# Kernel optimization log

Hardware: AMD Instinct MI355X
Metric: run time of the kernel (lower is better)

The kernel has to match this reference:

```python
import jax, jax.numpy as jnp
import numpy as np

N = 100_000   # nodes
E = 1_600_000 # edges per relation (avg degree 16)
IN, H, O = 128, 128, 128


def _graph_conv(x, src, dst, W, b, relu):
    """DGL GraphConv, norm='both': y = D_dst^{-1/2} A D_src^{-1/2} x W + b."""
    ones = jnp.ones(src.shape[0], dtype=x.dtype)
    deg_out = jnp.clip(jax.ops.segment_sum(ones, src, num_segments=N), 1.0)  # [N]
    deg_in = jnp.clip(jax.ops.segment_sum(ones, dst, num_segments=N), 1.0)   # [N]
    h = (x * (deg_out ** -0.5)[:, None]) @ W                 # [N, out] transform first (in==out)
    agg = jax.ops.segment_sum(h[src], dst, num_segments=N)   # SpMM: gather + scatter-add
    y = agg * (deg_in ** -0.5)[:, None] + b
    return jax.nn.relu(y) if relu else y


def setup_inputs() -> dict:
    key = jax.random.key(0)
    ks = jax.random.split(key, 8)
    g = 0.1  # weight scale ~ xavier for d=128
    return {
        "x": jax.random.normal(ks[0], (N, IN), dtype=jnp.float32),
        "src_i": jax.random.randint(ks[1], (E,), 0, N),
        "dst_i": jax.random.randint(ks[2], (E,), 0, N),
        "src_b": jax.random.randint(ks[3], (E,), 0, N),
        "dst_b": jax.random.randint(ks[4], (E,), 0, N),
        "W1_i": jax.random.normal(ks[5], (IN, H), dtype=jnp.float32) * g,
        "b1_i": jnp.zeros((H,), dtype=jnp.float32),
        "W1_b": jax.random.normal(ks[6], (IN, H), dtype=jnp.float32) * g,
        "b1_b": jnp.zeros((H,), dtype=jnp.float32),
        "W2": jax.random.normal(ks[7], (H, O), dtype=jnp.float32) * g,
        "b2": jnp.zeros((O,), dtype=jnp.float32),
    }


def reference(x, src_i, dst_i, src_b, dst_b, W1_i, b1_i, W1_b, b1_b, W2, b2):
    # conv1: HeteroGraphConv({'interacts','behave'}, aggregate='sum'), ReLU inside each conv
    h = (_graph_conv(x, src_i, dst_i, W1_i, b1_i, relu=True)
         + _graph_conv(x, src_b, dst_b, W1_b, b1_b, relu=True))
    # conv2: only 'interacts', no activation
    return _graph_conv(h, src_i, dst_i, W2, b2, relu=False)
```

## Files before the change

### kernel.cpp

```cpp
#include <hip/hip_runtime.h>
#include <hip/hip_fp16.h>

#define N_NODES 100000
#define N_EDGES 1600000
#define NT 98
#define XB 64
#define CHUNK (N_EDGES / XB)
#define HSH 2
#define HBINS (N_NODES / HSH)
#define FSH 8
#define FBINS (N_NODES / FSH)
#define WT_LD 136

typedef _Float16 half8_t __attribute__((ext_vector_type(8)));
typedef float f32x4 __attribute__((ext_vector_type(4)));

__device__ inline unsigned packh2(float a, float b) {
  __half2 h = __floats2half2_rn(a, b);
  return *(unsigned*)&h;
}

__global__ __launch_bounds__(256) void k_hist(
    const int* __restrict__ src_i, const int* __restrict__ dst_i,
    const int* __restrict__ src_b, const int* __restrict__ dst_b,
    unsigned* __restrict__ part32) {
  __shared__ unsigned h[HBINS / 4];
  const int xb = blockIdx.x, job = blockIdx.y, sl = blockIdx.z;
  const int* arr = (job == 0) ? src_i : (job == 1) ? dst_i : (job == 2) ? src_b : dst_b;
  const int lo = sl * HBINS;
  for (int i = threadIdx.x; i < HBINS / 4; i += 256) h[i] = 0;
  __syncthreads();
  const int4* a4 = (const int4*)(arr + xb * CHUNK);
  for (int q = threadIdx.x; q < CHUNK / 4; q += 256) {
    int4 v = a4[q];
    int t;
    t = v.x - lo; if ((unsigned)t < HBINS) atomicAdd(&h[t >> 2], 1u << ((t & 3) * 8));
    t = v.y - lo; if ((unsigned)t < HBINS) atomicAdd(&h[t >> 2], 1u << ((t & 3) * 8));
    t = v.z - lo; if ((unsigned)t < HBINS) atomicAdd(&h[t >> 2], 1u << ((t & 3) * 8));
    t = v.w - lo; if ((unsigned)t < HBINS) atomicAdd(&h[t >> 2], 1u << ((t & 3) * 8));
  }
  __syncthreads();
  unsigned* dst = part32 + ((size_t)(job * XB + xb) * N_NODES + lo) / 4;
  for (int i = threadIdx.x; i < HBINS / 4; i += 256) dst[i] = h[i];
}

__global__ __launch_bounds__(256) void k_hred(
    unsigned* __restrict__ part32, int* __restrict__ cnt_di_i, int* __restrict__ cnt_di_b,
    float* __restrict__ dso_i, float* __restrict__ dsi_i,
    float* __restrict__ dso_b, float* __restrict__ dsi_b) {
  const int b4 = blockIdx.x * 256 + threadIdx.x;
  if (b4 >= N_NODES / 4) return;
  const int b0 = b4 * 4;
  const size_t Q = N_NODES / 4;
  int s0, s1, s2, s3;
  s0 = s1 = s2 = s3 = 0;
  for (int xb = 0; xb < XB; ++xb) {
    unsigned w = part32[(size_t)(0 * XB + xb) * Q + b4];
    s0 += w & 255; s1 += (w >> 8) & 255; s2 += (w >> 16) & 255; s3 += w >> 24;
  }
  dso_i[b0] = rsqrtf((float)max(s0, 1)); dso_i[b0 + 1] = rsqrtf((float)max(s1, 1));
  dso_i[b0 + 2] = rsqrtf((float)max(s2, 1)); dso_i[b0 + 3] = rsqrtf((float)max(s3, 1));
  s0 = s1 = s2 = s3 = 0;
  for (int xb = 0; xb < XB; ++xb) {
    size_t idx = (size_t)(1 * XB + xb) * Q + b4;
    unsigned w = part32[idx];
    part32[idx] = (unsigned)s0 | ((unsigned)s1 << 8) | ((unsigned)s2 << 16) | ((unsigned)s3 << 24);
    s0 += w & 255; s1 += (w >> 8) & 255; s2 += (w >> 16) & 255; s3 += w >> 24;
  }
  cnt_di_i[b0] = s0; cnt_di_i[b0 + 1] = s1; cnt_di_i[b0 + 2] = s2; cnt_di_i[b0 + 3] = s3;
  dsi_i[b0] = rsqrtf((float)max(s0, 1)); dsi_i[b0 + 1] = rsqrtf((float)max(s1, 1));
  dsi_i[b0 + 2] = rsqrtf((float)max(s2, 1)); dsi_i[b0 + 3] = rsqrtf((float)max(s3, 1));
  s0 = s1 = s2 = s3 = 0;
  for (int xb = 0; xb < XB; ++xb) {
    unsigned w = part32[(size_t)(2 * XB + xb) * Q + b4];
    s0 += w & 255; s1 += (w >> 8) & 255; s2 += (w >> 16) & 255; s3 += w >> 24;
  }
  dso_b[b0] = rsqrtf((float)max(s0, 1)); dso_b[b0 + 1] = rsqrtf((float)max(s1, 1));
  dso_b[b0 + 2] = rsqrtf((float)max(s2, 1)); dso_b[b0 + 3] = rsqrtf((float)max(s3, 1));
  s0 = s1 = s2 = s3 = 0;
  for (int xb = 0; xb < XB; ++xb) {
    size_t idx = (size_t)(3 * XB + xb) * Q + b4;
    unsigned w = part32[idx];
    part32[idx] = (unsigned)s0 | ((unsigned)s1 << 8) | ((unsigned)s2 << 16) | ((unsigned)s3 << 24);
    s0 += w & 255; s1 += (w >> 8) & 255; s2 += (w >> 16) & 255; s3 += w >> 24;
  }
  cnt_di_b[b0] = s0; cnt_di_b[b0 + 1] = s1; cnt_di_b[b0 + 2] = s2; cnt_di_b[b0 + 3] = s3;
  dsi_b[b0] = rsqrtf((float)max(s0, 1)); dsi_b[b0 + 1] = rsqrtf((float)max(s1, 1));
  dsi_b[b0 + 2] = rsqrtf((float)max(s2, 1)); dsi_b[b0 + 3] = rsqrtf((float)max(s3, 1));
}

__global__ __launch_bounds__(256) void k_scan1(
    const int* __restrict__ cnt_i, const int* __restrict__ cnt_b,
    int* __restrict__ off_i, int* __restrict__ off_b, int* __restrict__ tsum) {
  const int rel = blockIdx.y;
  const int* cnt = rel ? cnt_b : cnt_i;
  int* off = rel ? off_b : off_i;
  const int tid = threadIdx.x;
  const int i0 = blockIdx.x * 1024 + tid * 4;
  int v[4];
#pragma unroll
  for (int k = 0; k < 4; ++k) v[k] = (i0 + k < N_NODES) ? cnt[i0 + k] : 0;
  int tl = v[0] + v[1] + v[2] + v[3];
  const int lane = tid & 63, wid = tid >> 6;
  int x = tl;
#pragma unroll
  for (int d = 1; d < 64; d <<= 1) {
    int t = __shfl_up(x, d);
    if (lane >= d) x += t;
  }
  __shared__ int wsum[4];
  if (lane == 63) wsum[wid] = x;
  __syncthreads();
  int wb = 0;
#pragma unroll
  for (int w = 0; w < 4; ++w)
    if (w < wid) wb += wsum[w];
  int run = wb + x - tl;
#pragma unroll
  for (int k = 0; k < 4; ++k) {
    if (i0 + k < N_NODES) off[i0 + k] = run;
    run += v[k];
  }
  if (tid == 255) tsum[rel * NT + blockIdx.x] = wb + x;
}

__global__ __launch_bounds__(256) void k_scan2(int* __restrict__ tsum) {
  __shared__ int a[256], b[256];
  const int t = threadIdx.x;
  for (int rel = 0; rel < 2; ++rel) {
    a[t] = (t < NT) ? tsum[rel * NT + t] : 0;
    __syncthreads();
    int* p = a;
    int* q = b;
    for (int d = 1; d < 256; d <<= 1) {
      q[t] = (t >= d) ? p[t - d] + p[t] : p[t];
      __syncthreads();
      int* tmp = p; p = q; q = tmp;
    }
    int excl = (t == 0) ? 0 : p[t - 1];
    if (t < NT) tsum[rel * NT + t] = excl;
    __syncthreads();
  }
}

__global__ __launch_bounds__(256) void k_scan3(
    const int* __restrict__ tsum, int* __restrict__ off_i, int* __restrict__ off_b) {
  const int rel = blockIdx.y;
  int* off = rel ? off_b : off_i;
  const int tb = tsum[rel * NT + blockIdx.x];
  const int i0 = blockIdx.x * 1024 + threadIdx.x * 4;
#pragma unroll
  for (int k = 0; k < 4; ++k)
    if (i0 + k < N_NODES) off[i0 + k] += tb;
  if (blockIdx.x == 0 && threadIdx.x == 0) off[N_NODES] = N_EDGES;
}

__global__ __launch_bounds__(256) void k_fill(
    const int* __restrict__ src_i, const int* __restrict__ dst_i,
    const int* __restrict__ src_b, const int* __restrict__ dst_b,
    const int* __restrict__ off_i, const int* __restrict__ off_b,
    const unsigned char* __restrict__ part8, int* __restrict__ es_i, int* __restrict__ es_b) {
  __shared__ int cur[FBINS];
  const int xb = blockIdx.x, rel = blockIdx.y, sl = blockIdx.z;
  const int* src = rel ? src_b : src_i;
  const int* dst = rel ? dst_b : dst_i;
  const int* off = rel ? off_b : off_i;
  int* es = rel ? es_b : es_i;
  const int lo = sl * FBINS;
  const unsigned char* pf = part8 + (size_t)((rel ? 3 : 1) * XB + xb) * N_NODES + lo;
  for (int i = threadIdx.x; i < FBINS; i += 256) cur[i] = off[lo + i] + pf[i];
  __syncthreads();
  const int4* s4p = (const int4*)(src + xb * CHUNK);
  const int4* d4p = (const int4*)(dst + xb * CHUNK);
  for (int q = threadIdx.x; q < CHUNK / 4; q += 256) {
    int4 d = d4p[q];
    int tx = d.x - lo, ty = d.y - lo, tz = d.z - lo, tw = d.w - lo;
    bool ax = (unsigned)tx < FBINS, ay = (unsigned)ty < FBINS,
         az = (unsigned)tz < FBINS, aw = (unsigned)tw < FBINS;
    if (!(ax | ay | az | aw)) continue;
    int4 s = s4p[q];
    if (ax) es[atomicAdd(&cur[tx], 1)] = s.x;
    if (ay) es[atomicAdd(&cur[ty], 1)] = s.y;
    if (az) es[atomicAdd(&cur[tz], 1)] = s.z;
    if (aw) es[atomicAdd(&cur[tw], 1)] = s.w;
  }
}

__global__ __launch_bounds__(256) void k_gemm_mfma(
    const float* __restrict__ A,
    const float* __restrict__ Wa, const float* __restrict__ Wb,
    const float* __restrict__ rsa, const float* __restrict__ rsb,
    unsigned short* __restrict__ Ca, unsigned short* __restrict__ Cb) {
  __shared__ unsigned short shw[128 * WT_LD];
  const int rel = blockIdx.y;
  const float* W = rel ? Wb : Wa;
  const float* rs = rel ? rsb : rsa;
  unsigned short* C = rel ? Cb : Ca;

  for (int t = threadIdx.x; t < 2048; t += 256) {
    int c4 = (t & 31) * 4;
    int k = (t >> 5) * 2;
    float4 w0 = *(const float4*)&W[k * 128 + c4];
    float4 w1 = *(const float4*)&W[(k + 1) * 128 + c4];
    *(unsigned*)&shw[(c4 + 0) * WT_LD + k] = packh2(w0.x, w1.x);
    *(unsigned*)&shw[(c4 + 1) * WT_LD + k] = packh2(w0.y, w1.y);
    *(unsigned*)&shw[(c4 + 2) * WT_LD + k] = packh2(w0.z, w1.z);
    *(unsigned*)&shw[(c4 + 3) * WT_LD + k] = packh2(w0.w, w1.w);
  }
  __syncthreads();

  const int w = threadIdx.x >> 6;
  const int l = threadIdx.x & 63;
  const int lc = l & 15;
  const int lk = l >> 4;
  const int rb = blockIdx.x * 128 + w * 32;

  f32x4 acc[2][8];
#pragma unroll
  for (int rf = 0; rf < 2; ++rf)
#pragma unroll
    for (int cf = 0; cf < 8; ++cf) acc[rf][cf] = (f32x4)(0.f);

  union H8 { unsigned u[4]; half8_t h; };

#pragma unroll
  for (int kc = 0; kc < 4; ++kc) {
    const int kbase = kc * 32 + lk * 8;
    H8 a[2];
#pragma unroll
    for (int rf = 0; rf < 2; ++rf) {
      int row = rb + rf * 16 + lc;
      row = min(row, N_NODES - 1);
      const float4* ap = (const float4*)(A + (size_t)row * 128 + kbase);
      float4 f0 = ap[0], f1 = ap[1];
      a[rf].u[0] = packh2(f0.x, f0.y);
      a[rf].u[1] = packh2(f0.z, f0.w);
      a[rf].u[2] = packh2(f1.x, f1.y);
      a[rf].u[3] = packh2(f1.z, f1.w);
    }
#pragma unroll
    for (int cf = 0; cf < 8; ++cf) {
      half8_t b = *(const half8_t*)&shw[(cf * 16 + lc) * WT_LD + kbase];
      acc[0][cf] = __builtin_amdgcn_mfma_f32_16x16x32_f16(a[0].h, b, acc[0][cf], 0, 0, 0);
      acc[1][cf] = __builtin_amdgcn_mfma_f32_16x16x32_f16(a[1].h, b, acc[1][cf], 0, 0, 0);
    }
  }

#pragma unroll
  for (int rf = 0; rf < 2; ++rf) {
#pragma unroll
    for (int reg = 0; reg < 4; ++reg) {
      int row = rb + rf * 16 + lk * 4 + reg;
      if (row < N_NODES) {
        float s = rs[row];
        unsigned short* crow = C + (size_t)row * 128 + lc;
#pragma unroll
        for (int cf = 0; cf < 8; ++cf) {
          __half h = __float2half_rn(acc[rf][cf][reg] * s);
          crow[cf * 16] = *(unsigned short*)&h;
        }
      }
    }
  }
}

template <int MODE>
__global__ __launch_bounds__(256) void k_spmm(
    const unsigned short* __restrict__ Xh, const int* __restrict__ off,
    const int* __restrict__ srcs, const float* __restrict__ dsi,
    const float* __restrict__ bias, float* __restrict__ out) {
  const int g = threadIdx.x >> 4;
  const int l = threadIdx.x & 15;
  const int n = blockIdx.x * 16 + g;
  if (n >= N_NODES) return;
  const int e0 = off[n];
  const int e1 = off[n + 1];
  const uint4* Xv = (const uint4*)Xh;
  float a0 = 0.f, a1 = 0.f, a2 = 0.f, a3 = 0.f, a4 = 0.f, a5 = 0.f, a6 = 0.f, a7 = 0.f;
  int e = e0;
  for (; e + 16 <= e1; e += 16) {
    int s = srcs[e + l];
    uint4 v[8];
#pragma unroll
    for (int j = 0; j < 8; ++j) v[j] = Xv[(size_t)__shfl(s, j, 16) * 16 + l];
#pragma unroll
    for (int j = 0; j < 8; ++j) {
      float2 f;
      f = __half22float2(*(__half2*)&v[j].x); a0 += f.x; a1 += f.y;
      f = __half22float2(*(__half2*)&v[j].y); a2 += f.x; a3 += f.y;
      f = __half22float2(*(__half2*)&v[j].z); a4 += f.x; a5 += f.y;
      f = __half22float2(*(__half2*)&v[j].w); a6 += f.x; a7 += f.y;
    }
#pragma unroll
    for (int j = 0; j < 8; ++j) v[j] = Xv[(size_t)__shfl(s, j + 8, 16) * 16 + l];
#pragma unroll
    for (int j = 0; j < 8; ++j) {
      float2 f;
      f = __half22float2(*(__half2*)&v[j].x); a0 += f.x; a1 += f.y;
      f = __half22float2(*(__half2*)&v[j].y); a2 += f.x; a3 += f.y;
      f = __half22float2(*(__half2*)&v[j].z); a4 += f.x; a5 += f.y;
      f = __half22float2(*(__half2*)&v[j].w); a6 += f.x; a7 += f.y;
    }
  }
  if (e < e1) {
    int s = (e + l < e1) ? srcs[e + l] : 0;
    int cnt = e1 - e;
    for (int j = 0; j < cnt; ++j) {
      uint4 v = Xv[(size_t)__shfl(s, j, 16) * 16 + l];
      float2 f;
      f = __half22float2(*(__half2*)&v.x); a0 += f.x; a1 += f.y;
      f = __half22float2(*(__half2*)&v.y); a2 += f.x; a3 += f.y;
      f = __half22float2(*(__half2*)&v.z); a4 += f.x; a5 += f.y;
      f = __half22float2(*(__half2*)&v.w); a6 += f.x; a7 += f.y;
    }
  }
  const float dn = dsi[n];
  float4 b0 = ((const float4*)bias)[l * 2];
  float4 b1 = ((const float4*)bias)[l * 2 + 1];
  float4 y0, y1;
  y0.x = fmaf(a0, dn, b0.x); y0.y = fmaf(a1, dn, b0.y);
  y0.z = fmaf(a2, dn, b0.z); y0.w = fmaf(a3, dn, b0.w);
  y1.x = fmaf(a4, dn, b1.x); y1.y = fmaf(a5, dn, b1.y);
  y1.z = fmaf(a6, dn, b1.z); y1.w = fmaf(a7, dn, b1.w);
  if (MODE != 2) {
    y0.x = fmaxf(y0.x, 0.f); y0.y = fmaxf(y0.y, 0.f);
    y0.z = fmaxf(y0.z, 0.f); y0.w = fmaxf(y0.w, 0.f);
    y1.x = fmaxf(y1.x, 0.f); y1.y = fmaxf(y1.y, 0.f);
    y1.z = fmaxf(y1.z, 0.f); y1.w = fmaxf(y1.w, 0.f);
  }
  float4* ov = (float4*)out;
  size_t oi = (size_t)n * 32 + l * 2;
  if (MODE == 1) {
    float4 p0 = ov[oi], p1 = ov[oi + 1];
    y0.x += p0.x; y0.y += p0.y; y0.z += p0.z; y0.w += p0.w;
    y1.x += p1.x; y1.y += p1.y; y1.z += p1.z; y1.w += p1.w;
  }
  ov[oi] = y0;
  ov[oi + 1] = y1;
}

extern "C" void kernel_launch(void* const* d_in, const int* in_sizes, int n_in,
                              void* d_out, int out_size, void* d_ws, size_t ws_size,
                              hipStream_t stream) {
  const float* x    = (const float*)d_in[0];
  const int* src_i  = (const int*)d_in[1];
  const int* dst_i  = (const int*)d_in[2];
  const int* src_b  = (const int*)d_in[3];
  const int* dst_b  = (const int*)d_in[4];
  const float* W1_i = (const float*)d_in[5];
  const float* b1_i = (const float*)d_in[6];
  const float* W1_b = (const float*)d_in[7];
  const float* b1_b = (const float*)d_in[8];
  const float* W2   = (const float*)d_in[9];
  const float* b2   = (const float*)d_in[10];
  float* out = (float*)d_out;

  char* ws = (char*)d_ws;
  size_t o = 0;
  auto alloc = [&](size_t bytes) {
    char* p = ws + o;
    o += (bytes + 255) & ~(size_t)255;
    return p;
  };
  float* dso_i = (float*)alloc(N_NODES * 4);
  float* dsi_i = (float*)alloc(N_NODES * 4);
  float* dso_b = (float*)alloc(N_NODES * 4);
  float* dsi_b = (float*)alloc(N_NODES * 4);
  int* cnt_di_i = (int*)alloc(N_NODES * 4);
  int* cnt_di_b = (int*)alloc(N_NODES * 4);
  int* off_i = (int*)alloc((N_NODES + 1) * 4);
  int* off_b = (int*)alloc((N_NODES + 1) * 4);
  int* tsum = (int*)alloc(2 * NT * 4);
  int* es_i = (int*)alloc((size_t)N_EDGES * 4);
  int* es_b = (int*)alloc((size_t)N_EDGES * 4);
  char* uni = alloc((size_t)2 * N_NODES * 128 * 2);
  unsigned* part32      = (unsigned*)uni;
  unsigned char* part8  = (unsigned char*)uni;
  unsigned short* buf_i = (unsigned short*)uni;
  unsigned short* buf_b = (unsigned short*)(uni + (size_t)N_NODES * 128 * 2);
  (void)ws_size; (void)in_sizes; (void)n_in; (void)out_size;

  k_hist<<<dim3(XB, 4, HSH), dim3(256), 0, stream>>>(src_i, dst_i, src_b, dst_b, part32);
  k_hred<<<(N_NODES / 4 + 255) / 256, dim3(256), 0, stream>>>(
      part32, cnt_di_i, cnt_di_b, dso_i, dsi_i, dso_b, dsi_b);
  k_scan1<<<dim3(NT, 2), dim3(256), 0, stream>>>(cnt_di_i, cnt_di_b, off_i, off_b, tsum);
  k_scan2<<<1, 256, 0, stream>>>(tsum);
  k_scan3<<<dim3(NT, 2), dim3(256), 0, stream>>>(tsum, off_i, off_b);
  k_fill<<<dim3(XB, 2, FSH), dim3(256), 0, stream>>>(
      src_i, dst_i, src_b, dst_b, off_i, off_b, part8, es_i, es_b);

  const int ggrid = (N_NODES + 127) / 128;
  const int sgrid = (N_NODES + 15) / 16;
  k_gemm_mfma<<<dim3(ggrid, 2), dim3(256), 0, stream>>>(
      x, W1_i, W1_b, dso_i, dso_b, buf_i, buf_b);
  k_spmm<0><<<sgrid, 256, 0, stream>>>(buf_i, off_i, es_i, dsi_i, b1_i, out);
  k_spmm<1><<<sgrid, 256, 0, stream>>>(buf_b, off_b, es_b, dsi_b, b1_b, out);
  k_gemm_mfma<<<dim3(ggrid, 1), dim3(256), 0, stream>>>(
      out, W2, W2, dso_i, dso_i, buf_i, buf_i);
  k_spmm<2><<<sgrid, 256, 0, stream>>>(buf_i, off_i, es_i, dsi_i, b2, out);
}
```

Baseline: 502.4 us.

## Replace multi-pass CSR fill with two-level bucket sort and fuse layer-1 SpMMs

The CSR build no longer rescans all edges once per destination slice. Edges are first bucketed by destination range into (dst,src) pairs using a shared-memory local sort and global bucket cursors. A per-bucket fill then scatters them into the CSR using LDS atomics. The two layer-1 SpMM kernels are fused into one kernel that computes both relations per node, avoiding a read-modify-write of the output. The gather unroll also grows to 16 loads in flight. The costs are an extra pairs buffer, more kernel launches, and non-deterministic edge order within each node.

```diff
diff --git a/kernel.cpp b/kernel.cpp
--- a/kernel.cpp
+++ b/kernel.cpp
@@ -8,12 +8,14 @@
 #define CHUNK (N_EDGES / XB)
 #define HSH 2
 #define HBINS (N_NODES / HSH)
-#define FSH 8
-#define FBINS (N_NODES / FSH)
+#define PSH 128
+#define PBINS ((N_NODES + PSH - 1) / PSH)
+#define TILE 4096
 #define WT_LD 136
 
 typedef _Float16 half8_t __attribute__((ext_vector_type(8)));
 typedef float f32x4 __attribute__((ext_vector_type(4)));
+typedef unsigned long long u64;
 
 __device__ inline unsigned packh2(float a, float b) {
   __half2 h = __floats2half2_rn(a, b);
@@ -45,7 +47,7 @@
 }
 
 __global__ __launch_bounds__(256) void k_hred(
-    unsigned* __restrict__ part32, int* __restrict__ cnt_di_i, int* __restrict__ cnt_di_b,
+    const unsigned* __restrict__ part32, int* __restrict__ cnt_di_i, int* __restrict__ cnt_di_b,
     float* __restrict__ dso_i, float* __restrict__ dsi_i,
     float* __restrict__ dso_b, float* __restrict__ dsi_b) {
   const int b4 = blockIdx.x * 256 + threadIdx.x;
@@ -62,9 +64,7 @@
   dso_i[b0 + 2] = rsqrtf((float)max(s2, 1)); dso_i[b0 + 3] = rsqrtf((float)max(s3, 1));
   s0 = s1 = s2 = s3 = 0;
   for (int xb = 0; xb < XB; ++xb) {
-    size_t idx = (size_t)(1 * XB + xb) * Q + b4;
-    unsigned w = part32[idx];
-    part32[idx] = (unsigned)s0 | ((unsigned)s1 << 8) | ((unsigned)s2 << 16) | ((unsigned)s3 << 24);
+    unsigned w = part32[(size_t)(1 * XB + xb) * Q + b4];
     s0 += w & 255; s1 += (w >> 8) & 255; s2 += (w >> 16) & 255; s3 += w >> 24;
   }
   cnt_di_i[b0] = s0; cnt_di_i[b0 + 1] = s1; cnt_di_i[b0 + 2] = s2; cnt_di_i[b0 + 3] = s3;
@@ -79,9 +79,7 @@
   dso_b[b0 + 2] = rsqrtf((float)max(s2, 1)); dso_b[b0 + 3] = rsqrtf((float)max(s3, 1));
   s0 = s1 = s2 = s3 = 0;
   for (int xb = 0; xb < XB; ++xb) {
-    size_t idx = (size_t)(3 * XB + xb) * Q + b4;
-    unsigned w = part32[idx];
-    part32[idx] = (unsigned)s0 | ((unsigned)s1 << 8) | ((unsigned)s2 << 16) | ((unsigned)s3 << 24);
+    unsigned w = part32[(size_t)(3 * XB + xb) * Q + b4];
     s0 += w & 255; s1 += (w >> 8) & 255; s2 += (w >> 16) & 255; s3 += w >> 24;
   }
   cnt_di_b[b0] = s0; cnt_di_b[b0 + 1] = s1; cnt_di_b[b0 + 2] = s2; cnt_di_b[b0 + 3] = s3;
@@ -155,34 +153,96 @@
   if (blockIdx.x == 0 && threadIdx.x == 0) off[N_NODES] = N_EDGES;
 }
 
-__global__ __launch_bounds__(256) void k_fill(
+__global__ void k_binit(const int* __restrict__ off_i, const int* __restrict__ off_b,
+                        int* __restrict__ bcur) {
+  int i = threadIdx.x;
+  if (i < 2 * PSH) {
+    int rel = i >> 7, b = i & (PSH - 1);
+    bcur[i] = (rel ? off_b : off_i)[b * PBINS];
+  }
+}
+
+__global__ __launch_bounds__(256) void k_bucket(
     const int* __restrict__ src_i, const int* __restrict__ dst_i,
     const int* __restrict__ src_b, const int* __restrict__ dst_b,
-    const int* __restrict__ off_i, const int* __restrict__ off_b,
-    const unsigned char* __restrict__ part8, int* __restrict__ es_i, int* __restrict__ es_b) {
-  __shared__ int cur[FBINS];
-  const int xb = blockIdx.x, rel = blockIdx.y, sl = blockIdx.z;
+    int* __restrict__ bcur, u64* __restrict__ pairs_i, u64* __restrict__ pairs_b) {
+  __shared__ u64 stage[TILE];
+  __shared__ int cnt[PSH], excl[PSH], gbase[PSH], lpos[PSH], sa[PSH], sb[PSH];
+  const int rel = blockIdx.y;
   const int* src = rel ? src_b : src_i;
   const int* dst = rel ? dst_b : dst_i;
+  u64* pairs = rel ? pairs_b : pairs_i;
+  const int tid = threadIdx.x;
+  const int base = blockIdx.x * TILE;
+  const int nE = min(TILE, N_EDGES - base);
+
+  for (int i = tid; i < PSH; i += 256) { cnt[i] = 0; lpos[i] = 0; }
+  __syncthreads();
+
+  u64 ed[16];
+  int eb[16];
+#pragma unroll
+  for (int j = 0; j < 16; ++j) {
+    int idx = base + j * 256 + tid;
+    if (idx < N_EDGES && (j * 256 + tid) < nE) {
+      int s = src[idx], d = dst[idx];
+      ed[j] = ((u64)(unsigned)d << 32) | (unsigned)s;
+      eb[j] = d / PBINS;
+      atomicAdd(&cnt[eb[j]], 1);
+    } else {
+      eb[j] = -1;
+    }
+  }
+  __syncthreads();
+  if (tid < PSH) sa[tid] = cnt[tid];
+  __syncthreads();
+  int* p = sa;
+  int* q = sb;
+  for (int d = 1; d < PSH; d <<= 1) {
+    if (tid < PSH) q[tid] = ((tid >= d) ? p[tid - d] : 0) + p[tid];
+    __syncthreads();
+    int* tmp = p; p = q; q = tmp;
+  }
+  if (tid < PSH) {
+    excl[tid] = p[tid] - cnt[tid];
+    gbase[tid] = atomicAdd(&bcur[rel * PSH + tid], cnt[tid]);
+  }
+  __syncthreads();
+#pragma unroll
+  for (int j = 0; j < 16; ++j) {
+    if (eb[j] >= 0) {
+      int pos = excl[eb[j]] + atomicAdd(&lpos[eb[j]], 1);
+      stage[pos] = ed[j];
+    }
+  }
+  __syncthreads();
+  for (int i = tid; i < nE; i += 256) {
+    u64 e = stage[i];
+    int b = (int)(e >> 32) / PBINS;
+    pairs[(size_t)gbase[b] + (i - excl[b])] = e;
+  }
+}
+
+__global__ __launch_bounds__(256) void k_fill2(
+    const int* __restrict__ off_i, const int* __restrict__ off_b,
+    const u64* __restrict__ pairs_i, const u64* __restrict__ pairs_b,
+    int* __restrict__ es_i, int* __restrict__ es_b) {
+  __shared__ int cur[PBINS];
+  const int b = blockIdx.x, rel = blockIdx.y;
   const int* off = rel ? off_b : off_i;
+  const u64* pairs = rel ? pairs_b : pairs_i;
   int* es = rel ? es_b : es_i;
-  const int lo = sl * FBINS;
-  const unsigned char* pf = part8 + (size_t)((rel ? 3 : 1) * XB + xb) * N_NODES + lo;
-  for (int i = threadIdx.x; i < FBINS; i += 256) cur[i] = off[lo + i] + pf[i];
-  __syncthreads();
-  const int4* s4p = (const int4*)(src + xb * CHUNK);
-  const int4* d4p = (const int4*)(dst + xb * CHUNK);
-  for (int q = threadIdx.x; q < CHUNK / 4; q += 256) {
-    int4 d = d4p[q];
-    int tx = d.x - lo, ty = d.y - lo, tz = d.z - lo, tw = d.w - lo;
-    bool ax = (unsigned)tx < FBINS, ay = (unsigned)ty < FBINS,
-         az = (unsigned)tz < FBINS, aw = (unsigned)tw < FBINS;
-    if (!(ax | ay | az | aw)) continue;
-    int4 s = s4p[q];
-    if (ax) es[atomicAdd(&cur[tx], 1)] = s.x;
-    if (ay) es[atomicAdd(&cur[ty], 1)] = s.y;
-    if (az) es[atomicAdd(&cur[tz], 1)] = s.z;
-    if (aw) es[atomicAdd(&cur[tw], 1)] = s.w;
+  const int lo = b * PBINS;
+  const int hi = min(lo + PBINS, N_NODES);
+  const int bins = hi - lo;
+  for (int i = threadIdx.x; i < bins; i += 256) cur[i] = off[lo + i];
+  __syncthreads();
+  const int p0 = off[lo], p1 = off[hi];
+  for (int idx = p0 + threadIdx.x; idx < p1; idx += 256) {
+    u64 e = pairs[idx];
+    int d = (int)(e >> 32);
+    int p = atomicAdd(&cur[d - lo], 1);
+    es[p] = (int)(unsigned)e;
   }
 }
 
@@ -264,8 +324,78 @@
   }
 }
 
-template <int MODE>
-__global__ __launch_bounds__(256) void k_spmm(
+__device__ inline void spmm_acc(const uint4* __restrict__ Xv, const int* __restrict__ srcs,
+                                int e0, int e1, int l, float* a) {
+  int e = e0;
+  for (; e + 16 <= e1; e += 16) {
+    int s = srcs[e + l];
+    uint4 v[16];
+#pragma unroll
+    for (int j = 0; j < 16; ++j) v[j] = Xv[(size_t)__shfl(s, j, 16) * 16 + l];
+#pragma unroll
+    for (int j = 0; j < 16; ++j) {
+      float2 f;
+      f = __half22float2(*(__half2*)&v[j].x); a[0] += f.x; a[1] += f.y;
+      f = __half22float2(*(__half2*)&v[j].y); a[2] += f.x; a[3] += f.y;
+      f = __half22float2(*(__half2*)&v[j].z); a[4] += f.x; a[5] += f.y;
+      f = __half22float2(*(__half2*)&v[j].w); a[6] += f.x; a[7] += f.y;
+    }
+  }
+  if (e < e1) {
+    int s = (e + l < e1) ? srcs[e + l] : 0;
+    int cnt = e1 - e;
+    for (int j = 0; j < cnt; ++j) {
+      uint4 v = Xv[(size_t)__shfl(s, j, 16) * 16 + l];
+      float2 f;
+      f = __half22float2(*(__half2*)&v.x); a[0] += f.x; a[1] += f.y;
+      f = __half22float2(*(__half2*)&v.y); a[2] += f.x; a[3] += f.y;
+      f = __half22float2(*(__half2*)&v.z); a[4] += f.x; a[5] += f.y;
+      f = __half22float2(*(__half2*)&v.w); a[6] += f.x; a[7] += f.y;
+    }
+  }
+}
+
+__global__ __launch_bounds__(256) void k_spmm_l1(
+    const unsigned short* __restrict__ Xi, const int* __restrict__ off_i,
+    const int* __restrict__ es_i, const float* __restrict__ dsi_i,
+    const float* __restrict__ b_i,
+    const unsigned short* __restrict__ Xb, const int* __restrict__ off_b,
+    const int* __restrict__ es_b, const float* __restrict__ dsi_b,
+    const float* __restrict__ b_b, float* __restrict__ out) {
+  const int g = threadIdx.x >> 4;
+  const int l = threadIdx.x & 15;
+  const int n = blockIdx.x * 16 + g;
+  if (n >= N_NODES) return;
+  float y[8];
+  {
+    float a[8] = {0.f, 0.f, 0.f, 0.f, 0.f, 0.f, 0.f, 0.f};
+    spmm_acc((const uint4*)Xi, es_i, off_i[n], off_i[n + 1], l, a);
+    const float dn = dsi_i[n];
+    float4 c0 = ((const float4*)b_i)[l * 2];
+    float4 c1 = ((const float4*)b_i)[l * 2 + 1];
+    y[0] = fmaxf(fmaf(a[0], dn, c0.x), 0.f); y[1] = fmaxf(fmaf(a[1], dn, c0.y), 0.f);
+    y[2] = fmaxf(fmaf(a[2], dn, c0.z), 0.f); y[3] = fmaxf(fmaf(a[3], dn, c0.w), 0.f);
+    y[4] = fmaxf(fmaf(a[4], dn, c1.x), 0.f); y[5] = fmaxf(fmaf(a[5], dn, c1.y), 0.f);
+    y[6] = fmaxf(fmaf(a[6], dn, c1.z), 0.f); y[7] = fmaxf(fmaf(a[7], dn, c1.w), 0.f);
+  }
+  {
+    float a[8] = {0.f, 0.f, 0.f, 0.f, 0.f, 0.f, 0.f, 0.f};
+    spmm_acc((const uint4*)Xb, es_b, off_b[n], off_b[n + 1], l, a);
+    const float dn = dsi_b[n];
+    float4 c0 = ((const float4*)b_b)[l * 2];
+    float4 c1 = ((const float4*)b_b)[l * 2 + 1];
+    y[0] += fmaxf(fmaf(a[0], dn, c0.x), 0.f); y[1] += fmaxf(fmaf(a[1], dn, c0.y), 0.f);
+    y[2] += fmaxf(fmaf(a[2], dn, c0.z), 0.f); y[3] += fmaxf(fmaf(a[3], dn, c0.w), 0.f);
+    y[4] += fmaxf(fmaf(a[4], dn, c1.x), 0.f); y[5] += fmaxf(fmaf(a[5], dn, c1.y), 0.f);
+    y[6] += fmaxf(fmaf(a[6], dn, c1.z), 0.f); y[7] += fmaxf(fmaf(a[7], dn, c1.w), 0.f);
+  }
+  float4* ov = (float4*)out;
+  size_t oi = (size_t)n * 32 + l * 2;
+  ov[oi] = make_float4(y[0], y[1], y[2], y[3]);
+  ov[oi + 1] = make_float4(y[4], y[5], y[6], y[7]);
+}
+
+__global__ __launch_bounds__(256) void k_spmm_l2(
     const unsigned short* __restrict__ Xh, const int* __restrict__ off,
     const int* __restrict__ srcs, const float* __restrict__ dsi,
     const float* __restrict__ bias, float* __restrict__ out) {
@@ -273,68 +403,18 @@
   const int l = threadIdx.x & 15;
   const int n = blockIdx.x * 16 + g;
   if (n >= N_NODES) return;
-  const int e0 = off[n];
-  const int e1 = off[n + 1];
-  const uint4* Xv = (const uint4*)Xh;
-  float a0 = 0.f, a1 = 0.f, a2 = 0.f, a3 = 0.f, a4 = 0.f, a5 = 0.f, a6 = 0.f, a7 = 0.f;
-  int e = e0;
-  for (; e + 16 <= e1; e += 16) {
-    int s = srcs[e + l];
-    uint4 v[8];
-#pragma unroll
-    for (int j = 0; j < 8; ++j) v[j] = Xv[(size_t)__shfl(s, j, 16) * 16 + l];
-#pragma unroll
-    for (int j = 0; j < 8; ++j) {
-      float2 f;
-      f = __half22float2(*(__half2*)&v[j].x); a0 += f.x; a1 += f.y;
-      f = __half22float2(*(__half2*)&v[j].y); a2 += f.x; a3 += f.y;
-      f = __half22float2(*(__half2*)&v[j].z); a4 += f.x; a5 += f.y;
-      f = __half22float2(*(__half2*)&v[j].w); a6 += f.x; a7 += f.y;
-    }
-#pragma unroll
-    for (int j = 0; j < 8; ++j) v[j] = Xv[(size_t)__shfl(s, j + 8, 16) * 16 + l];
-#pragma unroll
-    for (int j = 0; j < 8; ++j) {
-      float2 f;
-      f = __half22float2(*(__half2*)&v[j].x); a0 += f.x; a1 += f.y;
-      f = __half22float2(*(__half2*)&v[j].y); a2 += f.x; a3 += f.y;
-      f = __half22float2(*(__half2*)&v[j].z); a4 += f.x; a5 += f.y;
-      f = __half22float2(*(__half2*)&v[j].w); a6 += f.x; a7 += f.y;
-    }
-  }
-  if (e < e1) {
-    int s = (e + l < e1) ? srcs[e + l] : 0;
-    int cnt = e1 - e;
-    for (int j = 0; j < cnt; ++j) {
-      uint4 v = Xv[(size_t)__shfl(s, j, 16) * 16 + l];
-      float2 f;
-      f = __half22float2(*(__half2*)&v.x); a0 += f.x; a1 += f.y;
-      f = __half22float2(*(__half2*)&v.y); a2 += f.x; a3 += f.y;
-      f = __half22float2(*(__half2*)&v.z); a4 += f.x; a5 += f.y;
-      f = __half22float2(*(__half2*)&v.w); a6 += f.x; a7 += f.y;
-    }
-  }
+  float a[8] = {0.f, 0.f, 0.f, 0.f, 0.f, 0.f, 0.f, 0.f};
+  spmm_acc((const uint4*)Xh, srcs, off[n], off[n + 1], l, a);
   const float dn = dsi[n];
-  float4 b0 = ((const float4*)bias)[l * 2];
-  float4 b1 = ((const float4*)bias)[l * 2 + 1];
+  float4 c0 = ((const float4*)bias)[l * 2];
+  float4 c1 = ((const float4*)bias)[l * 2 + 1];
   float4 y0, y1;
-  y0.x = fmaf(a0, dn, b0.x); y0.y = fmaf(a1, dn, b0.y);
-  y0.z = fmaf(a2, dn, b0.z); y0.w = fmaf(a3, dn, b0.w);
-  y1.x = fmaf(a4, dn, b1.x); y1.y = fmaf(a5, dn, b1.y);
-  y1.z = fmaf(a6, dn, b1.z); y1.w = fmaf(a7, dn, b1.w);
-  if (MODE != 2) {
-    y0.x = fmaxf(y0.x, 0.f); y0.y = fmaxf(y0.y, 0.f);
-    y0.z = fmaxf(y0.z, 0.f); y0.w = fmaxf(y0.w, 0.f);
-    y1.x = fmaxf(y1.x, 0.f); y1.y = fmaxf(y1.y, 0.f);
-    y1.z = fmaxf(y1.z, 0.f); y1.w = fmaxf(y1.w, 0.f);
-  }
+  y0.x = fmaf(a[0], dn, c0.x); y0.y = fmaf(a[1], dn, c0.y);
+  y0.z = fmaf(a[2], dn, c0.z); y0.w = fmaf(a[3], dn, c0.w);
+  y1.x = fmaf(a[4], dn, c1.x); y1.y = fmaf(a[5], dn, c1.y);
+  y1.z = fmaf(a[6], dn, c1.z); y1.w = fmaf(a[7], dn, c1.w);
   float4* ov = (float4*)out;
   size_t oi = (size_t)n * 32 + l * 2;
-  if (MODE == 1) {
-    float4 p0 = ov[oi], p1 = ov[oi + 1];
-    y0.x += p0.x; y0.y += p0.y; y0.z += p0.z; y0.w += p0.w;
-    y1.x += p1.x; y1.y += p1.y; y1.z += p1.z; y1.w += p1.w;
-  }
   ov[oi] = y0;
   ov[oi + 1] = y1;
 }
@@ -371,11 +451,13 @@
   int* off_i = (int*)alloc((N_NODES + 1) * 4);
   int* off_b = (int*)alloc((N_NODES + 1) * 4);
   int* tsum = (int*)alloc(2 * NT * 4);
+  int* bcur = (int*)alloc(2 * PSH * 4);
   int* es_i = (int*)alloc((size_t)N_EDGES * 4);
   int* es_b = (int*)alloc((size_t)N_EDGES * 4);
   char* uni = alloc((size_t)2 * N_NODES * 128 * 2);
   unsigned* part32      = (unsigned*)uni;
-  unsigned char* part8  = (unsigned char*)uni;
+  u64* pairs_i          = (u64*)uni;
+  u64* pairs_b          = pairs_i + N_EDGES;
   unsigned short* buf_i = (unsigned short*)uni;
   unsigned short* buf_b = (unsigned short*)(uni + (size_t)N_NODES * 128 * 2);
   (void)ws_size; (void)in_sizes; (void)n_in; (void)out_size;
@@ -386,16 +468,19 @@
   k_scan1<<<dim3(NT, 2), dim3(256), 0, stream>>>(cnt_di_i, cnt_di_b, off_i, off_b, tsum);
   k_scan2<<<1, 256, 0, stream>>>(tsum);
   k_scan3<<<dim3(NT, 2), dim3(256), 0, stream>>>(tsum, off_i, off_b);
-  k_fill<<<dim3(XB, 2, FSH), dim3(256), 0, stream>>>(
-      src_i, dst_i, src_b, dst_b, off_i, off_b, part8, es_i, es_b);
+  k_binit<<<1, 256, 0, stream>>>(off_i, off_b, bcur);
+  k_bucket<<<dim3((N_EDGES + TILE - 1) / TILE, 2), dim3(256), 0, stream>>>(
+      src_i, dst_i, src_b, dst_b, bcur, pairs_i, pairs_b);
+  k_fill2<<<dim3(PSH, 2), dim3(256), 0, stream>>>(
+      off_i, off_b, pairs_i, pairs_b, es_i, es_b);
 
   const int ggrid = (N_NODES + 127) / 128;
   const int sgrid = (N_NODES + 15) / 16;
   k_gemm_mfma<<<dim3(ggrid, 2), dim3(256), 0, stream>>>(
       x, W1_i, W1_b, dso_i, dso_b, buf_i, buf_b);
-  k_spmm<0><<<sgrid, 256, 0, stream>>>(buf_i, off_i, es_i, dsi_i, b1_i, out);
-  k_spmm<1><<<sgrid, 256, 0, stream>>>(buf_b, off_b, es_b, dsi_b, b1_b, out);
+  k_spmm_l1<<<sgrid, 256, 0, stream>>>(
+      buf_i, off_i, es_i, dsi_i, b1_i, buf_b, off_b, es_b, dsi_b, b1_b, out);
   k_gemm_mfma<<<dim3(ggrid, 1), dim3(256), 0, stream>>>(
       out, W2, W2, dso_i, dso_i, buf_i, buf_i);
-  k_spmm<2><<<sgrid, 256, 0, stream>>>(buf_i, off_i, es_i, dsi_i, b2, out);
-}
+  k_spmm_l2<<<sgrid, 256, 0, stream>>>(buf_i, off_i, es_i, dsi_i, b2, out);
+}
```

Result: faster. 466.5 us (-7.1%).
